# Optimization experiments

Hardware: AMD Instinct MI355X
Metric: run time of the kernel (lower is better)

Reference implementation:

```python
import jax, jax.numpy as jnp
import numpy as np

N_NODES = 10000
N_EDGES = 640000
IN_CH = 128
HID = 256
OUT_CH = 10
NUM_GRAPHS = 64
EPS = 0.0  # non-trainable buffer, initial_eps=0


def setup_inputs() -> dict:
    key = jax.random.key(0)
    ks = jax.random.split(key, 12)
    x = jax.random.normal(ks[0], (N_NODES, IN_CH), dtype=jnp.float32)
    edge_index = jax.random.randint(ks[1], (2, N_EDGES), 0, N_NODES, dtype=jnp.int64)
    batch = jnp.sort(jax.random.randint(ks[2], (N_NODES,), 0, NUM_GRAPHS, dtype=jnp.int64))
    edge_weights = jax.random.uniform(ks[3], (N_EDGES,), dtype=jnp.float32)
    def lin(k, fan_in, fan_out):
        bound = 1.0 / np.sqrt(fan_in)
        kw, kb = jax.random.split(k)
        W = jax.random.uniform(kw, (fan_out, fan_in), minval=-bound, maxval=bound, dtype=jnp.float32)
        b = jax.random.uniform(kb, (fan_out,), minval=-bound, maxval=bound, dtype=jnp.float32)
        return W, b
    W1, b1 = lin(ks[4], IN_CH, HID)
    W2, b2 = lin(ks[5], HID, HID)
    W3, b3 = lin(ks[6], HID, HID)
    Wl, bl = lin(ks[7], HID, OUT_CH)
    return {"x": x, "edge_index": edge_index, "batch": batch, "edge_weights": edge_weights,
            "W1": W1, "b1": b1, "W2": W2, "b2": b2, "W3": W3, "b3": b3, "Wl": Wl, "bl": bl}


def _ginw_conv(x, edge_index, edge_weights, W, b):
    # message: edge_weight * x_j (source nodes), aggregated by add at target i
    src, dst = edge_index[0], edge_index[1]
    msg = edge_weights[:, None] * x[src]           # [E, F]
    agg = jax.ops.segment_sum(msg, dst, num_segments=N_NODES)  # [N, F]
    out = agg + (1.0 + EPS) * x
    return out @ W.T + b


def reference(x, edge_index, batch, edge_weights, W1, b1, W2, b2, W3, b3, Wl, bl):
    h = jax.nn.relu(_ginw_conv(x, edge_index, edge_weights, W1, b1))
    h = jax.nn.relu(_ginw_conv(h, edge_index, edge_weights, W2, b2))
    h = jax.nn.relu(_ginw_conv(h, edge_index, edge_weights, W3, b3))
    # global mean pool over graphs
    sums = jax.ops.segment_sum(h, batch, num_segments=NUM_GRAPHS)        # [G, HID]
    cnts = jax.ops.segment_sum(jnp.ones((N_NODES,), h.dtype), batch, num_segments=NUM_GRAPHS)
    pooled = sums / jnp.maximum(cnts, 1.0)[:, None]
    return pooled @ Wl.T + bl
```

## Files before the change

kernel.cpp:

```cpp
#include <hip/hip_runtime.h>
#include <hip/hip_fp16.h>

namespace {
constexpr int NN   = 10000;
constexpr int NE   = 640000;
constexpr int INC  = 128;
constexpr int HIDC = 256;
constexpr int OUTC = 10;
constexpr int NG   = 64;
constexpr int PP   = 8;

constexpr int NB     = 157;
constexpr int G1     = 64;
constexpr int CHUNK1 = NE / G1;
constexpr int CAPB   = 128;
}

typedef __attribute__((ext_vector_type(8))) short short8;
typedef __attribute__((ext_vector_type(4))) float f32x4;

__device__ __forceinline__ ushort f2bf(float f) {
    uint u = __float_as_uint(f);
    uint r = u + 0x7FFFu + ((u >> 16) & 1u);
    return (ushort)(r >> 16);
}
__device__ __forceinline__ float bf2f(ushort u) {
    return __uint_as_float(((uint)u) << 16);
}
__device__ __forceinline__ float rec_w(uint rec) {
    return __half2float(__ushort_as_half((ushort)(rec & 0xFFFFu)));
}

__global__ __launch_bounds__(256) void f2bf_kernel(const float* __restrict__ in,
                                                   ushort* __restrict__ out, int n4) {
    int i = blockIdx.x * blockDim.x + threadIdx.x;
    if (i >= n4) return;
    float4 v = ((const float4*)in)[i];
    ushort4 o;
    o.x = f2bf(v.x); o.y = f2bf(v.y); o.z = f2bf(v.z); o.w = f2bf(v.w);
    ((ushort4*)out)[i] = o;
}

__global__ __launch_bounds__(256) void partition_kernel(const int* __restrict__ ei,
                                                        const float* __restrict__ ew,
                                                        uint2* __restrict__ stag,
                                                        int* __restrict__ cnts) {
    __shared__ int lcnt[NB];
    const int t = threadIdx.x, g = blockIdx.x;
    for (int i = t; i < NB; i += 256) lcnt[i] = 0;
    __syncthreads();
    const int base = g * CHUNK1;
    for (int i = t; i < CHUNK1; i += 256) {
        const int e = base + i;
        const int dst = ei[NE + e];
        const int src = ei[e];
        const ushort hw = __half_as_ushort(__float2half(ew[e]));
        const int bk = dst >> 6;
        const int idx = atomicAdd(&lcnt[bk], 1);
        if (idx < CAPB)
            stag[((size_t)g * NB + bk) * CAPB + idx] =
                make_uint2(((uint)src << 16) | (uint)hw, (uint)dst);
    }
    __syncthreads();
    for (int i = t; i < NB; i += 256) cnts[g * NB + i] = min(lcnt[i], CAPB);
}

__global__ __launch_bounds__(256) void bucketscan_kernel(const int* __restrict__ cnts,
                                                         int* __restrict__ bucket_start,
                                                         int* __restrict__ row_start) {
    __shared__ int part[256];
    const int t = threadIdx.x;
    int s = 0;
    if (t < NB)
        for (int g = 0; g < G1; g++) s += cnts[g * NB + t];
    part[t] = s;
    __syncthreads();
    for (int off = 1; off < 256; off <<= 1) {
        int v = (t >= off) ? part[t - off] : 0;
        __syncthreads();
        part[t] += v;
        __syncthreads();
    }
    if (t < NB) bucket_start[t] = part[t] - s;
    if (t == 0) {
        bucket_start[NB] = part[255];
        row_start[NN] = part[255];
    }
}

__global__ __launch_bounds__(256) void place_kernel(const uint2* __restrict__ stag,
                                                    const int* __restrict__ cnts,
                                                    const int* __restrict__ bucket_start,
                                                    int* __restrict__ row_start,
                                                    uint* __restrict__ erec) {
    const int b = blockIdx.x;
    const int t = threadIdx.x;
    __shared__ int part[256];
    __shared__ int foff[G1 + 1];
    __shared__ int h[64];
    __shared__ int curl[64];

    const int c = (t < G1) ? cnts[t * NB + b] : 0;
    part[t] = c;
    __syncthreads();
    for (int off = 1; off < 256; off <<= 1) {
        int v = (t >= off) ? part[t - off] : 0;
        __syncthreads();
        part[t] += v;
        __syncthreads();
    }
    if (t < G1) foff[t] = part[t] - c;
    if (t == 0) foff[G1] = part[255];
    if (t < 64) h[t] = 0;
    __syncthreads();
    const int Rb = foff[G1];

    for (int r = t; r < Rb; r += 256) {
        int lo = 0, hi = G1;
        while (hi - lo > 1) { int mid = (lo + hi) >> 1; if (foff[mid] <= r) lo = mid; else hi = mid; }
        uint2 rec = stag[((size_t)lo * NB + b) * CAPB + (r - foff[lo])];
        atomicAdd(&h[rec.y & 63], 1);
    }
    __syncthreads();

    const int hv = (t < 64) ? h[t] : 0;
    part[t] = hv;
    __syncthreads();
    for (int off = 1; off < 256; off <<= 1) {
        int v = (t >= off) ? part[t - off] : 0;
        __syncthreads();
        part[t] += v;
        __syncthreads();
    }
    const int bs = bucket_start[b];
    if (t < 64) {
        const int excl = part[t] - hv;
        const int node = b * 64 + t;
        if (node < NN) row_start[node] = bs + excl;
        curl[t] = excl;
    }
    __syncthreads();

    for (int r = t; r < Rb; r += 256) {
        int lo = 0, hi = G1;
        while (hi - lo > 1) { int mid = (lo + hi) >> 1; if (foff[mid] <= r) lo = mid; else hi = mid; }
        uint2 rec = stag[((size_t)lo * NB + b) * CAPB + (r - foff[lo])];
        const int pos = bs + atomicAdd(&curl[rec.y & 63], 1);
        erec[pos] = rec.x;
    }
}

template <int F>
__global__ __launch_bounds__(256) void gather_bf16_kernel(const int* __restrict__ row_start,
                                                          const uint* __restrict__ erec,
                                                          const ushort* __restrict__ x,
                                                          ushort* __restrict__ out) {
    constexpr int VEC = F / 64;
    constexpr int U = 12;
    const int n = blockIdx.x * 4 + (threadIdx.x >> 6);
    const int lane = threadIdx.x & 63;
    if (n >= NN) return;
    const int beg = row_start[n];
    const int end = row_start[n + 1];
    const size_t loff = (size_t)lane * VEC;

    float acc[VEC];
    {
        ushort v[VEC];
        if (VEC == 4) *(ushort4*)v = *(const ushort4*)(x + (size_t)n * F + loff);
        else          *(ushort2*)v = *(const ushort2*)(x + (size_t)n * F + loff);
#pragma unroll
        for (int i = 0; i < VEC; i++) acc[i] = bf2f(v[i]);
    }

    int e = beg;
    for (; e + U <= end; e += U) {
        uint rec[U];
#pragma unroll
        for (int u = 0; u < U; u++) rec[u] = erec[e + u];
        ushort v[U][VEC];
#pragma unroll
        for (int u = 0; u < U; u++) {
            const ushort* r = x + (size_t)(rec[u] >> 16) * F + loff;
            if (VEC == 4) *(ushort4*)v[u] = *(const ushort4*)r;
            else          *(ushort2*)v[u] = *(const ushort2*)r;
        }
#pragma unroll
        for (int u = 0; u < U; u++) {
            const float w = rec_w(rec[u]);
#pragma unroll
            for (int i = 0; i < VEC; i++) acc[i] += w * bf2f(v[u][i]);
        }
    }
    for (; e < end; e++) {
        uint rec = erec[e];
        const float w = rec_w(rec);
        ushort v[VEC];
        const ushort* r = x + (size_t)(rec >> 16) * F + loff;
        if (VEC == 4) *(ushort4*)v = *(const ushort4*)r;
        else          *(ushort2*)v = *(const ushort2*)r;
#pragma unroll
        for (int i = 0; i < VEC; i++) acc[i] += w * bf2f(v[i]);
    }

    ushort o[VEC];
#pragma unroll
    for (int i = 0; i < VEC; i++) o[i] = f2bf(acc[i]);
    if (VEC == 4) *(ushort4*)(out + (size_t)n * F + loff) = *(ushort4*)o;
    else          *(ushort2*)(out + (size_t)n * F + loff) = *(ushort2*)o;
}

template <int K>
__global__ __launch_bounds__(256) void mfma_gemm_kernel(const ushort* __restrict__ A,
                                                        const float* __restrict__ W,
                                                        const float* __restrict__ bias,
                                                        ushort* __restrict__ C, int M) {
    constexpr int LDW = K + 8;
    __shared__ ushort Ws[64 * LDW];
    const int tid = threadIdx.x;
    const int bm = blockIdx.x * 128;
    const int bn = blockIdx.y * 64;

    constexpr int CPR = K / 4;
    for (int idx = tid; idx < 64 * CPR; idx += 256) {
        int r = idx / CPR, c = idx % CPR;
        float4 v = *(const float4*)(W + (size_t)(bn + r) * K + c * 4);
        ushort4 o;
        o.x = f2bf(v.x); o.y = f2bf(v.y); o.z = f2bf(v.z); o.w = f2bf(v.w);
        *(ushort4*)(&Ws[r * LDW + c * 4]) = o;
    }
    __syncthreads();

    const int wave = tid >> 6;
    const int lane = tid & 63;
    const int lrow = lane & 15;
    const int lq   = lane >> 4;
    const int m0 = bm + wave * 32;

    f32x4 acc[2][4] = {};
    const int r0 = min(m0 + lrow, M - 1);
    const int r1 = min(m0 + 16 + lrow, M - 1);

    for (int k0 = 0; k0 < K; k0 += 32) {
        const int kk = k0 + lq * 8;
        short8 a0 = *(const short8*)(A + (size_t)r0 * K + kk);
        short8 a1 = *(const short8*)(A + (size_t)r1 * K + kk);
        short8 b[4];
#pragma unroll
        for (int j = 0; j < 4; j++)
            b[j] = *(const short8*)(&Ws[(j * 16 + lrow) * LDW + kk]);
#pragma unroll
        for (int j = 0; j < 4; j++) {
            acc[0][j] = __builtin_amdgcn_mfma_f32_16x16x32_bf16(a0, b[j], acc[0][j], 0, 0, 0);
            acc[1][j] = __builtin_amdgcn_mfma_f32_16x16x32_bf16(a1, b[j], acc[1][j], 0, 0, 0);
        }
    }

#pragma unroll
    for (int sub = 0; sub < 2; sub++) {
#pragma unroll
        for (int j = 0; j < 4; j++) {
            const int gn = bn + j * 16 + lrow;
            const float bv = bias[gn];
#pragma unroll
            for (int i = 0; i < 4; i++) {
                const int gm = m0 + sub * 16 + lq * 4 + i;
                if (gm < M) {
                    float v = acc[sub][j][i] + bv;
                    v = fmaxf(v, 0.0f);
                    C[(size_t)gm * HIDC + gn] = f2bf(v);
                }
            }
        }
    }
}

__device__ __forceinline__ int lower_bound_batch(const int* __restrict__ batch, int val) {
    int lo = 0, hi = NN;
    while (lo < hi) {
        int mid = (lo + hi) >> 1;
        if (batch[mid] < val) lo = mid + 1;
        else hi = mid;
    }
    return lo;
}

__global__ __launch_bounds__(256) void pool_partial_kernel(const ushort* __restrict__ h,
                                                           const int* __restrict__ batch,
                                                           float* __restrict__ partials) {
    const int g = blockIdx.x;
    const int p = blockIdx.y;
    const int c = threadIdx.x;
    const int lo = lower_bound_batch(batch, g);
    const int hi = lower_bound_batch(batch, g + 1);
    const int cnt = hi - lo;
    const int chunk = (cnt + PP - 1) / PP;
    const int n0 = lo + p * chunk;
    const int n1 = min(hi, n0 + chunk);
    float sum = 0.0f;
    for (int n = n0; n < n1; n++) sum += bf2f(h[(size_t)n * HIDC + c]);
    partials[((size_t)g * PP + p) * HIDC + c] = sum;
}

__global__ __launch_bounds__(256) void head_kernel(const float* __restrict__ partials,
                                                   const int* __restrict__ batch,
                                                   const float* __restrict__ Wl,
                                                   const float* __restrict__ bl,
                                                   float* __restrict__ out) {
    __shared__ float s[HIDC];
    const int g = blockIdx.x;
    const int c = threadIdx.x;
    const int lo = lower_bound_batch(batch, g);
    const int hi = lower_bound_batch(batch, g + 1);
    const float inv = 1.0f / fmaxf((float)(hi - lo), 1.0f);
    float sum = 0.0f;
#pragma unroll
    for (int p = 0; p < PP; p++) sum += partials[((size_t)g * PP + p) * HIDC + c];
    s[c] = sum * inv;
    __syncthreads();
    if (c < OUTC) {
        float acc = bl[c];
        for (int k = 0; k < HIDC; k++) acc += s[k] * Wl[(size_t)c * HIDC + k];
        out[(size_t)g * OUTC + c] = acc;
    }
}

extern "C" void kernel_launch(void* const* d_in, const int* in_sizes, int n_in,
                              void* d_out, int out_size, void* d_ws, size_t ws_size,
                              hipStream_t stream) {
    const float* x     = (const float*)d_in[0];
    const int*   ei    = (const int*)d_in[1];
    const int*   batch = (const int*)d_in[2];
    const float* ew    = (const float*)d_in[3];
    const float* W1    = (const float*)d_in[4];
    const float* b1    = (const float*)d_in[5];
    const float* W2    = (const float*)d_in[6];
    const float* b2    = (const float*)d_in[7];
    const float* W3    = (const float*)d_in[8];
    const float* b3    = (const float*)d_in[9];
    const float* Wl    = (const float*)d_in[10];
    const float* bl    = (const float*)d_in[11];

    char* p = (char*)d_ws;
    uint2* stag = (uint2*)p;
    ushort* xb     = (ushort*)p;
    ushort* agg128 = xb + (size_t)NN * INC;
    ushort* agg256 = (ushort*)p;
    p += (size_t)G1 * NB * CAPB * 8;
    ushort* h      = (ushort*)p; p += (size_t)NN * HIDC * 2;
    uint*   erec   = (uint*)p;   p += (size_t)NE * 4;
    float*  partials = (float*)p; p += (size_t)NG * PP * HIDC * 4;
    int*    cnts   = (int*)p;    p += (size_t)G1 * NB * 4;
    int*    bucket_start = (int*)p; p += (NB + 1) * 4 + 12;
    int*    row_start = (int*)p; p += 40016;

    partition_kernel<<<G1, 256, 0, stream>>>(ei, ew, stag, cnts);
    bucketscan_kernel<<<1, 256, 0, stream>>>(cnts, bucket_start, row_start);
    place_kernel<<<NB, 256, 0, stream>>>(stag, cnts, bucket_start, row_start, erec);

    f2bf_kernel<<<(NN * INC / 4 + 255) / 256, 256, 0, stream>>>(x, xb, NN * INC / 4);

    const int gather_grid = (NN + 3) / 4;
    dim3 gemm_grid((NN + 127) / 128, HIDC / 64);

    gather_bf16_kernel<INC><<<gather_grid, 256, 0, stream>>>(row_start, erec, xb, agg128);
    mfma_gemm_kernel<INC><<<gemm_grid, 256, 0, stream>>>(agg128, W1, b1, h, NN);

    gather_bf16_kernel<HIDC><<<gather_grid, 256, 0, stream>>>(row_start, erec, h, agg256);
    mfma_gemm_kernel<HIDC><<<gemm_grid, 256, 0, stream>>>(agg256, W2, b2, h, NN);

    gather_bf16_kernel<HIDC><<<gather_grid, 256, 0, stream>>>(row_start, erec, h, agg256);
    mfma_gemm_kernel<HIDC><<<gemm_grid, 256, 0, stream>>>(agg256, W3, b3, h, NN);

    pool_partial_kernel<<<dim3(NG, PP), 256, 0, stream>>>(h, batch, partials);
    head_kernel<<<NG, 256, 0, stream>>>(partials, batch, Wl, bl, (float*)d_out);
}
```

Before: 277.9 us.

## Widen edge partition grid, fuse bf16 cast, cache staged records in LDS

Raises the partition grid from 64 to 256 blocks with smaller per-bucket capacity, folds the x-to-bf16 conversion into the partition kernel to drop a launch, and writes a transposed count array so the bucket scan reads contiguous int4 rows. The place kernel keeps the first LCAP staged records in shared memory, so its second pass avoids the binary search and the global reread. The 40KB LDS array may lower occupancy in place_kernel. CAPB=64 per (block, bucket) must still hold the roughly 16 expected edges each, otherwise edges are dropped.

```diff
diff --git a/kernel.cpp b/kernel.cpp
--- a/kernel.cpp
+++ b/kernel.cpp
@@ -11,9 +11,10 @@
 constexpr int PP   = 8;
 
 constexpr int NB     = 157;
-constexpr int G1     = 64;
+constexpr int G1     = 256;
 constexpr int CHUNK1 = NE / G1;
-constexpr int CAPB   = 128;
+constexpr int CAPB   = 64;
+constexpr int LCAP   = 5120;
 }
 
 typedef __attribute__((ext_vector_type(8))) short short8;
@@ -31,20 +32,13 @@
     return __half2float(__ushort_as_half((ushort)(rec & 0xFFFFu)));
 }
 
-__global__ __launch_bounds__(256) void f2bf_kernel(const float* __restrict__ in,
-                                                   ushort* __restrict__ out, int n4) {
-    int i = blockIdx.x * blockDim.x + threadIdx.x;
-    if (i >= n4) return;
-    float4 v = ((const float4*)in)[i];
-    ushort4 o;
-    o.x = f2bf(v.x); o.y = f2bf(v.y); o.z = f2bf(v.z); o.w = f2bf(v.w);
-    ((ushort4*)out)[i] = o;
-}
-
 __global__ __launch_bounds__(256) void partition_kernel(const int* __restrict__ ei,
                                                         const float* __restrict__ ew,
                                                         uint2* __restrict__ stag,
-                                                        int* __restrict__ cnts) {
+                                                        int* __restrict__ cnts,
+                                                        int* __restrict__ cnts_T,
+                                                        const float* __restrict__ x,
+                                                        ushort* __restrict__ xb) {
     __shared__ int lcnt[NB];
     const int t = threadIdx.x, g = blockIdx.x;
     for (int i = t; i < NB; i += 256) lcnt[i] = 0;
@@ -62,17 +56,34 @@
                 make_uint2(((uint)src << 16) | (uint)hw, (uint)dst);
     }
     __syncthreads();
-    for (int i = t; i < NB; i += 256) cnts[g * NB + i] = min(lcnt[i], CAPB);
-}
-
-__global__ __launch_bounds__(256) void bucketscan_kernel(const int* __restrict__ cnts,
+    for (int i = t; i < NB; i += 256) {
+        const int c = min(lcnt[i], CAPB);
+        cnts[g * NB + i] = c;
+        cnts_T[i * G1 + g] = c;
+    }
+    const int total4 = NN * INC / 4;
+    for (int i = g * 256 + t; i < total4; i += G1 * 256) {
+        float4 v = ((const float4*)x)[i];
+        ushort4 o;
+        o.x = f2bf(v.x); o.y = f2bf(v.y); o.z = f2bf(v.z); o.w = f2bf(v.w);
+        ((ushort4*)xb)[i] = o;
+    }
+}
+
+__global__ __launch_bounds__(256) void bucketscan_kernel(const int* __restrict__ cnts_T,
                                                          int* __restrict__ bucket_start,
                                                          int* __restrict__ row_start) {
     __shared__ int part[256];
     const int t = threadIdx.x;
     int s = 0;
-    if (t < NB)
-        for (int g = 0; g < G1; g++) s += cnts[g * NB + t];
+    if (t < NB) {
+        const int4* r = (const int4*)(cnts_T + (size_t)t * G1);
+#pragma unroll 8
+        for (int i = 0; i < G1 / 4; i++) {
+            int4 v = r[i];
+            s += v.x + v.y + v.z + v.w;
+        }
+    }
     part[t] = s;
     __syncthreads();
     for (int off = 1; off < 256; off <<= 1) {
@@ -99,9 +110,11 @@
     __shared__ int foff[G1 + 1];
     __shared__ int h[64];
     __shared__ int curl[64];
-
-    const int c = (t < G1) ? cnts[t * NB + b] : 0;
+    __shared__ uint2 srec[LCAP];
+
+    const int c = cnts[t * NB + b];
     part[t] = c;
+    if (t < 64) h[t] = 0;
     __syncthreads();
     for (int off = 1; off < 256; off <<= 1) {
         int v = (t >= off) ? part[t - off] : 0;
@@ -109,9 +122,8 @@
         part[t] += v;
         __syncthreads();
     }
-    if (t < G1) foff[t] = part[t] - c;
-    if (t == 0) foff[G1] = part[255];
-    if (t < 64) h[t] = 0;
+    foff[t] = part[t] - c;
+    if (t == 255) foff[G1] = part[255];
     __syncthreads();
     const int Rb = foff[G1];
 
@@ -119,6 +131,7 @@
         int lo = 0, hi = G1;
         while (hi - lo > 1) { int mid = (lo + hi) >> 1; if (foff[mid] <= r) lo = mid; else hi = mid; }
         uint2 rec = stag[((size_t)lo * NB + b) * CAPB + (r - foff[lo])];
+        if (r < LCAP) srec[r] = rec;
         atomicAdd(&h[rec.y & 63], 1);
     }
     __syncthreads();
@@ -142,9 +155,13 @@
     __syncthreads();
 
     for (int r = t; r < Rb; r += 256) {
-        int lo = 0, hi = G1;
-        while (hi - lo > 1) { int mid = (lo + hi) >> 1; if (foff[mid] <= r) lo = mid; else hi = mid; }
-        uint2 rec = stag[((size_t)lo * NB + b) * CAPB + (r - foff[lo])];
+        uint2 rec;
+        if (r < LCAP) rec = srec[r];
+        else {
+            int lo = 0, hi = G1;
+            while (hi - lo > 1) { int mid = (lo + hi) >> 1; if (foff[mid] <= r) lo = mid; else hi = mid; }
+            rec = stag[((size_t)lo * NB + b) * CAPB + (r - foff[lo])];
+        }
         const int pos = bs + atomicAdd(&curl[rec.y & 63], 1);
         erec[pos] = rec.x;
     }
@@ -342,23 +359,21 @@
     const float* bl    = (const float*)d_in[11];
 
     char* p = (char*)d_ws;
-    uint2* stag = (uint2*)p;
-    ushort* xb     = (ushort*)p;
-    ushort* agg128 = xb + (size_t)NN * INC;
-    ushort* agg256 = (ushort*)p;
-    p += (size_t)G1 * NB * CAPB * 8;
+    uint2*  stag   = (uint2*)p;  p += (size_t)G1 * NB * CAPB * 8;
+    ushort* xb     = (ushort*)p; p += (size_t)NN * INC * 2;
+    ushort* agg128 = (ushort*)p; p += (size_t)NN * INC * 2;
+    ushort* agg256 = (ushort*)p; p += (size_t)NN * HIDC * 2;
     ushort* h      = (ushort*)p; p += (size_t)NN * HIDC * 2;
     uint*   erec   = (uint*)p;   p += (size_t)NE * 4;
     float*  partials = (float*)p; p += (size_t)NG * PP * HIDC * 4;
     int*    cnts   = (int*)p;    p += (size_t)G1 * NB * 4;
-    int*    bucket_start = (int*)p; p += (NB + 1) * 4 + 12;
+    int*    cnts_T = (int*)p;    p += (size_t)NB * G1 * 4;
+    int*    bucket_start = (int*)p; p += 1024;
     int*    row_start = (int*)p; p += 40016;
 
-    partition_kernel<<<G1, 256, 0, stream>>>(ei, ew, stag, cnts);
-    bucketscan_kernel<<<1, 256, 0, stream>>>(cnts, bucket_start, row_start);
+    partition_kernel<<<G1, 256, 0, stream>>>(ei, ew, stag, cnts, cnts_T, x, xb);
+    bucketscan_kernel<<<1, 256, 0, stream>>>(cnts_T, bucket_start, row_start);
     place_kernel<<<NB, 256, 0, stream>>>(stag, cnts, bucket_start, row_start, erec);
-
-    f2bf_kernel<<<(NN * INC / 4 + 255) / 256, 256, 0, stream>>>(x, xb, NN * INC / 4);
 
     const int gather_grid = (NN + 3) / 4;
     dim3 gemm_grid((NN + 127) / 128, HIDC / 64);
```

Measured after the change: 261.4 us. 5.9% less time.
